# Performance work log

Hardware: AMD Instinct MI355X
Metric: run time of the kernel (lower is better)

## Reference

```python
import jax, jax.numpy as jnp
import numpy as np

CONF_THRES = 0.25   # NMS.conf
IOU_THRES = 0.45    # NMS.iou
MAX_NMS = 1024      # fixed candidate count so greedy NMS is jit-compatible
IMG = 640.0


def setup_inputs() -> dict:
    key = jax.random.key(0)
    k0, k1, k2, k3, k4 = jax.random.split(key, 5)
    B, N = 32, 25200
    cxcy = jax.random.uniform(k0, (B, N, 2), dtype=jnp.float32) * IMG
    wh = jax.random.uniform(k1, (B, N, 2), dtype=jnp.float32) * 80.0 + 2.0
    obj = jax.random.uniform(k2, (B, N, 1), dtype=jnp.float32)
    lmk = jax.random.uniform(k3, (B, N, 10), dtype=jnp.float32) * IMG
    cls = jax.random.uniform(k4, (B, N, 1), dtype=jnp.float32)
    # layout: [cx, cy, w, h, obj, 10 landmark coords, 1 class score]
    prediction = jnp.concatenate([cxcy, wh, obj, lmk, cls], axis=2)
    return {"prediction": prediction}


def xywh2xyxy(x):
    cx, cy, w, h = x[:, 0], x[:, 1], x[:, 2], x[:, 3]
    return jnp.stack([cx - w / 2, cy - h / 2, cx + w / 2, cy + h / 2], axis=1)


def pairwise_iou(b):  # b: [K,4] xyxy -> [K,K]
    area = (b[:, 2] - b[:, 0]) * (b[:, 3] - b[:, 1])
    lt = jnp.maximum(b[:, None, :2], b[None, :, :2])
    rb = jnp.minimum(b[:, None, 2:], b[None, :, 2:])
    wh = jnp.clip(rb - lt, 0.0)
    inter = wh[..., 0] * wh[..., 1]
    return inter / (area[:, None] + area[None, :] - inter + 1e-7)


def _nms_image(pred):  # pred: [N,16]
    obj = pred[:, 4]
    score = pred[:, 15] * obj  # x[:,15:] *= x[:,4:5]; nc==1 -> single class, j==0
    valid = (obj > CONF_THRES) & (score > CONF_THRES)  # xc filter + conf filter
    s = jnp.where(valid, score, -1.0)
    top_s, idx = jax.lax.top_k(s, MAX_NMS)  # score-sorted candidates (greedy NMS order)
    x = pred[idx]  # [K,16]
    box = xywh2xyxy(x[:, :4])
    vmask = top_s > 0.0  # valid candidates (invalid slots carry score -1)
    # class offset c = j*4096 is identically 0 since nc==1 -> skip
    iou = pairwise_iou(box)  # [K,K]
    rng = jnp.arange(MAX_NMS)

    def step(keep, i):
        sup = keep[i] & (iou[i] > IOU_THRES) & (rng > i)
        return keep & ~sup, None

    keep, _ = jax.lax.scan(step, vmask, rng)
    det = jnp.concatenate(
        [box, top_s[:, None], x[:, 5:15], jnp.zeros((MAX_NMS, 1), pred.dtype)], axis=1
    )  # [K,16] = box(4) | conf(1) | landmarks(10) | class(1)=0
    return det * keep[:, None].astype(det.dtype), keep


def reference(prediction):
    # Fixed-shape analogue of the per-image ragged output: detections padded to
    # MAX_NMS rows per image (zeroed where suppressed) plus a keep mask.
    det, keep = jax.vmap(_nms_image)(prediction)
    return det, keep
```

## Files before the change

### kernel.cpp

```cpp
#include <hip/hip_runtime.h>
#include <stdint.h>

#define NB 32
#define NN 25200
#define NN4 6300
#define TOPK 1024
#define NF 16
#define CONF 0.25f
#define IOU_T 0.45f
#define NBIN 4096
#define CAP 2048
#define KEY_BASE 0xBE800001u

__device__ __forceinline__ uint32_t score_key(float obj, float cls) {
  float score = __fmul_rn(cls, obj);
  bool valid = (obj > CONF) && (score > CONF);
  float s = valid ? score : -1.0f;
  uint32_t u = __float_as_uint(s);
  return (u & 0x80000000u) ? ~u : (u | 0x80000000u);
}

__device__ __forceinline__ uint64_t shfl_xor_u64(uint64_t v, int m) {
  uint32_t lo = __shfl_xor((uint32_t)v, m, 64);
  uint32_t hi = __shfl_xor((uint32_t)(v >> 32), m, 64);
  return ((uint64_t)hi << 32) | lo;
}

__global__ void k_keys(const float* __restrict__ pred, uint32_t* __restrict__ keys) {
  int g = blockIdx.x * blockDim.x + threadIdx.x;
  if (g >= NB * NN) return;
  const float* row = pred + (size_t)g * NF;
  keys[g] = score_key(row[4], row[15]);
}

__global__ __launch_bounds__(1024) void k_select(const uint32_t* __restrict__ keys,
                                                 int* __restrict__ sel) {
  int b = blockIdx.x;
  int tid = threadIdx.x;
  int lane = tid & 63, wid = tid >> 6;
  const uint4* kb4 = (const uint4*)(keys + (size_t)b * NN);
  __shared__ uint32_t hist[NBIN];
  __shared__ uint64_t ent[CAP];
  __shared__ uint32_t wsum[16];
  __shared__ uint32_t sh_bin;
  __shared__ uint32_t sh_cnt;
  #pragma unroll
  for (int k = 0; k < 4; ++k) hist[tid + 1024 * k] = 0;
  ent[tid] = 0; ent[tid + 1024] = 0;
  if (tid == 0) { sh_cnt = 0; sh_bin = 0; }
  __syncthreads();

  uint4 kreg[7];
  #pragma unroll
  for (int k = 0; k < 7; ++k) {
    int i = tid + k * 1024;
    if (i < NN4) {
      kreg[k] = kb4[i];
      uint32_t kv[4] = {kreg[k].x, kreg[k].y, kreg[k].z, kreg[k].w};
      #pragma unroll
      for (int c = 0; c < 4; ++c) {
        uint32_t key = kv[c];
        if (key >= KEY_BASE) {
          uint32_t bin = (key - KEY_BASE) >> 12;
          if (bin > NBIN - 1) bin = NBIN - 1;
          atomicAdd(&hist[bin], 1u);
        }
      }
    }
  }
  __syncthreads();

  uint32_t h[4]; uint32_t s = 0;
  #pragma unroll
  for (int k = 0; k < 4; ++k) { h[k] = hist[NBIN - 1 - (4 * tid + k)]; s += h[k]; }
  uint32_t my = s;
  #pragma unroll
  for (int d = 1; d < 64; d <<= 1) {
    uint32_t v = __shfl_up(s, d, 64);
    if (lane >= d) s += v;
  }
  if (lane == 63) wsum[wid] = s;
  __syncthreads();
  uint32_t base = 0;
  for (int w = 0; w < wid; ++w) base += wsum[w];
  uint32_t cum = base + s - my;
  #pragma unroll
  for (int k = 0; k < 4; ++k) {
    if (cum < TOPK && cum + h[k] >= TOPK) sh_bin = (uint32_t)(NBIN - 1 - (4 * tid + k));
    cum += h[k];
  }
  __syncthreads();
  uint32_t thr = KEY_BASE + (sh_bin << 12);

  #pragma unroll
  for (int k = 0; k < 7; ++k) {
    int i = tid + k * 1024;
    if (i < NN4) {
      uint32_t kv[4] = {kreg[k].x, kreg[k].y, kreg[k].z, kreg[k].w};
      #pragma unroll
      for (int c = 0; c < 4; ++c) {
        uint32_t key = kv[c];
        if (key >= thr) {
          uint32_t p = atomicAdd(&sh_cnt, 1u);
          if (p < CAP) ent[p] = ((uint64_t)key << 32) | (uint32_t)(~(uint32_t)(4 * i + c));
        }
      }
    }
  }
  __syncthreads();

  uint64_t v0 = ent[tid], v1 = ent[tid + 1024];
  for (unsigned kk = 2; kk <= CAP; kk <<= 1) {
    for (unsigned j = kk >> 1; j > 0; j >>= 1) {
      if (j == 1024) {
        uint64_t mx = v0 > v1 ? v0 : v1;
        uint64_t mn = v0 > v1 ? v1 : v0;
        v0 = mx; v1 = mn;
      } else if (j >= 64) {
        __syncthreads();
        ent[tid] = v0; ent[tid + 1024] = v1;
        __syncthreads();
        uint64_t p0 = ent[tid ^ j], p1 = ent[(tid ^ j) + 1024];
        bool low = ((tid & j) == 0);
        bool d0 = ((tid & kk) == 0);
        bool d1 = (((tid + 1024) & kk) == 0);
        v0 = (low != d0) ? (v0 < p0 ? v0 : p0) : (v0 > p0 ? v0 : p0);
        v1 = (low != d1) ? (v1 < p1 ? v1 : p1) : (v1 > p1 ? v1 : p1);
      } else {
        uint64_t p0 = shfl_xor_u64(v0, (int)j);
        uint64_t p1 = shfl_xor_u64(v1, (int)j);
        bool low = ((tid & j) == 0);
        bool d0 = ((tid & kk) == 0);
        bool d1 = (((tid + 1024) & kk) == 0);
        v0 = (low != d0) ? (v0 < p0 ? v0 : p0) : (v0 > p0 ? v0 : p0);
        v1 = (low != d1) ? (v1 < p1 ? v1 : p1) : (v1 > p1 ? v1 : p1);
      }
    }
  }
  uint32_t n = ~(uint32_t)(v0 & 0xFFFFFFFFu);
  if (n >= NN) n = 0;
  sel[(size_t)b * TOPK + tid] = (int)n;
}

__global__ __launch_bounds__(1024) void k_mask(const float* __restrict__ pred,
                                               const int* __restrict__ sel,
                                               uint32_t* __restrict__ mask) {
  int b = blockIdx.x;
  int sblk = blockIdx.y;
  int tid = threadIdx.x;
  int rg = tid & 31;
  int cc = tid >> 5;
  __shared__ float bx1[TOPK], by1[TOPK], bx2[TOPK], by2[TOPK], bar[TOPK];
  {
    int n = sel[(size_t)b * TOPK + tid];
    const float4* row = (const float4*)(pred + ((size_t)b * NN + n) * NF);
    float4 r0 = row[0];
    float hw = __fmul_rn(r0.z, 0.5f), hh = __fmul_rn(r0.w, 0.5f);
    float x1 = __fsub_rn(r0.x, hw), y1 = __fsub_rn(r0.y, hh);
    float x2 = __fadd_rn(r0.x, hw), y2 = __fadd_rn(r0.y, hh);
    bx1[tid] = x1; by1[tid] = y1; bx2[tid] = x2; by2[tid] = y2;
    bar[tid] = __fmul_rn(__fsub_rn(x2, x1), __fsub_rn(y2, y1));
  }
  __syncthreads();
  int i0 = sblk * 128 + rg * 4;
  int iw = i0 >> 5;
  uint32_t wreg[4] = {0u, 0u, 0u, 0u};
  if (cc >= iw) {
    float rx1[4], ry1[4], rx2[4], ry2[4], rar[4];
    #pragma unroll
    for (int k = 0; k < 4; ++k) {
      rx1[k] = bx1[i0 + k]; ry1[k] = by1[i0 + k];
      rx2[k] = bx2[i0 + k]; ry2[k] = by2[i0 + k]; rar[k] = bar[i0 + k];
    }
    for (int jj = 0; jj < 32; ++jj) {
      int j = cc * 32 + jj;
      float cx1 = bx1[j], cy1 = by1[j], cx2 = bx2[j], cy2 = by2[j], car = bar[j];
      #pragma unroll
      for (int k = 0; k < 4; ++k) {
        float lx = fmaxf(rx1[k], cx1);
        float ly = fmaxf(ry1[k], cy1);
        float rx = fminf(rx2[k], cx2);
        float ry = fminf(ry2[k], cy2);
        float wd = fmaxf(__fsub_rn(rx, lx), 0.0f);
        float ht = fmaxf(__fsub_rn(ry, ly), 0.0f);
        float inter = __fmul_rn(wd, ht);
        float den = __fadd_rn(__fsub_rn(__fadd_rn(rar[k], car), inter), 1e-7f);
        float iou = __fdiv_rn(inter, den);
        wreg[k] |= (iou > IOU_T ? 1u : 0u) << jj;
      }
    }
    if (cc == iw) {
      #pragma unroll
      for (int k = 0; k < 4; ++k)
        wreg[k] &= ~((2u << ((i0 + k) & 31)) - 1u);
    }
  }
  uint4 out = make_uint4(wreg[0], wreg[1], wreg[2], wreg[3]);
  *(uint4*)&mask[((size_t)b * 32 + cc) * TOPK + i0] = out;
}

__global__ __launch_bounds__(1024, 4) void k_scan_out(const float* __restrict__ pred,
                                                      const int* __restrict__ sel,
                                                      const uint32_t* __restrict__ mask,
                                                      float* __restrict__ det,
                                                      float* __restrict__ keep_out) {
  int b = blockIdx.x;
  int tid = threadIdx.x;
  int lane = tid & 63, wv = tid >> 6;
  __shared__ uint32_t vbits[32];
  __shared__ uint32_t keepw[32];

  uint32_t cur[32];
  const uint4* mc = nullptr;
  if (tid < 32) {
    mc = (const uint4*)(mask + (size_t)b * (32 * TOPK) + (size_t)tid * TOPK);
    #pragma unroll
    for (int q = 0; q < 8; ++q) *(uint4*)&cur[4 * q] = mc[q];
  }

  int n = sel[(size_t)b * TOPK + tid];
  const float4* rowv = (const float4*)(pred + ((size_t)b * NN + n) * NF);
  float4 r0 = rowv[0], r1 = rowv[1], r2 = rowv[2], r3 = rowv[3];
  float obj = r1.x, cls = r3.w;
  float score = __fmul_rn(cls, obj);
  bool valid = (obj > CONF) && (score > CONF);
  uint64_t bal = __ballot(valid);
  if (lane == 0) {
    vbits[2 * wv] = (uint32_t)bal;
    vbits[2 * wv + 1] = (uint32_t)(bal >> 32);
  }
  __syncthreads();

  if (tid < 32) {
    int l = tid;
    uint32_t kw = vbits[l];
    uint32_t nxt[32];
    for (int w = 0; w < 32; ++w) {
      if (w < 31) {
        #pragma unroll
        for (int q = 0; q < 8; ++q) *(uint4*)&nxt[4 * q] = mc[(w + 1) * 8 + q];
      }
      uint32_t rw = kw;
      #pragma unroll
      for (int t = 0; t < 32; ++t)
        if ((rw >> t) & 1u) rw &= ~cur[t];
      uint32_t rf = __shfl(rw, w, 64);
      if (l == w) {
        kw = rf;
      } else if (l > w) {
        uint32_t acc = 0;
        #pragma unroll
        for (int t = 0; t < 32; ++t) acc |= ((rf >> t) & 1u) ? cur[t] : 0u;
        kw &= ~acc;
      }
      if (w < 31) {
        #pragma unroll
        for (int t = 0; t < 32; ++t) cur[t] = nxt[t];
      }
    }
    keepw[l] = kw;
  }
  __syncthreads();

  bool kept = (keepw[tid >> 5] >> (tid & 31)) & 1u;
  float m = kept ? 1.0f : 0.0f;
  float hw = __fmul_rn(r0.z, 0.5f), hh = __fmul_rn(r0.w, 0.5f);
  float4 o0 = make_float4(__fsub_rn(r0.x, hw) * m, __fsub_rn(r0.y, hh) * m,
                          __fadd_rn(r0.x, hw) * m, __fadd_rn(r0.y, hh) * m);
  float4 o1 = make_float4(score * m, r1.y * m, r1.z * m, r1.w * m);
  float4 o2 = make_float4(r2.x * m, r2.y * m, r2.z * m, r2.w * m);
  float4 o3 = make_float4(r3.x * m, r3.y * m, r3.z * m, 0.0f);
  float4* dst = (float4*)(det + ((size_t)b * TOPK + tid) * NF);
  dst[0] = o0; dst[1] = o1; dst[2] = o2; dst[3] = o3;
  keep_out[(size_t)b * TOPK + tid] = m;
}

extern "C" void kernel_launch(void* const* d_in, const int* in_sizes, int n_in,
                              void* d_out, int out_size, void* d_ws, size_t ws_size,
                              hipStream_t stream) {
  const float* pred = (const float*)d_in[0];
  float* det = (float*)d_out;
  float* keep = det + (size_t)NB * TOPK * NF;

  uint8_t* ws = (uint8_t*)d_ws;
  uint32_t* keys = (uint32_t*)ws;
  int* sel = (int*)(ws + (size_t)NB * NN * 4);
  uint32_t* mask = (uint32_t*)(ws + (size_t)NB * NN * 4
                                  + (size_t)NB * TOPK * 4);

  k_keys<<<(NB * NN + 255) / 256, 256, 0, stream>>>(pred, keys);
  k_select<<<NB, 1024, 0, stream>>>(keys, sel);
  dim3 gm(NB, 8);
  k_mask<<<gm, 1024, 0, stream>>>(pred, sel, mask);
  k_scan_out<<<NB, 1024, 0, stream>>>(pred, sel, mask, det, keep);
}
```

Baseline: 167.3 us.

## Fuse IoU mask and greedy scan kernels using per-image atomic counter handoff

```diff
diff --git a/kernel.cpp b/kernel.cpp
--- a/kernel.cpp
+++ b/kernel.cpp
@@ -26,7 +26,9 @@
   return ((uint64_t)hi << 32) | lo;
 }
 
-__global__ void k_keys(const float* __restrict__ pred, uint32_t* __restrict__ keys) {
+__global__ void k_keys(const float* __restrict__ pred, uint32_t* __restrict__ keys,
+                       uint32_t* __restrict__ cnt) {
+  if (blockIdx.x == 0 && threadIdx.x < NB) cnt[threadIdx.x] = 0u;
   int g = blockIdx.x * blockDim.x + threadIdx.x;
   if (g >= NB * NN) return;
   const float* row = pred + (size_t)g * NF;
@@ -142,15 +144,21 @@
   sel[(size_t)b * TOPK + tid] = (int)n;
 }
 
-__global__ __launch_bounds__(1024) void k_mask(const float* __restrict__ pred,
-                                               const int* __restrict__ sel,
-                                               uint32_t* __restrict__ mask) {
+__global__ __launch_bounds__(1024, 4) void k_maskscan(const float* __restrict__ pred,
+                                                      const int* __restrict__ sel,
+                                                      uint32_t* __restrict__ mask,
+                                                      uint32_t* __restrict__ cnt,
+                                                      float* __restrict__ det,
+                                                      float* __restrict__ keep_out) {
   int b = blockIdx.x;
   int sblk = blockIdx.y;
   int tid = threadIdx.x;
   int rg = tid & 31;
   int cc = tid >> 5;
   __shared__ float bx1[TOPK], by1[TOPK], bx2[TOPK], by2[TOPK], bar[TOPK];
+  __shared__ uint32_t vbits[32];
+  __shared__ uint32_t keepw[32];
+
   {
     int n = sel[(size_t)b * TOPK + tid];
     const float4* row = (const float4*)(pred + ((size_t)b * NN + n) * NF);
@@ -197,26 +205,17 @@
   }
   uint4 out = make_uint4(wreg[0], wreg[1], wreg[2], wreg[3]);
   *(uint4*)&mask[((size_t)b * 32 + cc) * TOPK + i0] = out;
-}
-
-__global__ __launch_bounds__(1024, 4) void k_scan_out(const float* __restrict__ pred,
-                                                      const int* __restrict__ sel,
-                                                      const uint32_t* __restrict__ mask,
-                                                      float* __restrict__ det,
-                                                      float* __restrict__ keep_out) {
-  int b = blockIdx.x;
-  int tid = threadIdx.x;
+
+  __threadfence();
+  __syncthreads();
+  if (tid == 0)
+    __hip_atomic_fetch_add(&cnt[b], 1u, __ATOMIC_RELEASE, __HIP_MEMORY_SCOPE_AGENT);
+  if (sblk != 0) return;
+
   int lane = tid & 63, wv = tid >> 6;
-  __shared__ uint32_t vbits[32];
-  __shared__ uint32_t keepw[32];
-
-  uint32_t cur[32];
   const uint4* mc = nullptr;
-  if (tid < 32) {
+  if (tid < 32)
     mc = (const uint4*)(mask + (size_t)b * (32 * TOPK) + (size_t)tid * TOPK);
-    #pragma unroll
-    for (int q = 0; q < 8; ++q) *(uint4*)&cur[4 * q] = mc[q];
-  }
 
   int n = sel[(size_t)b * TOPK + tid];
   const float4* rowv = (const float4*)(pred + ((size_t)b * NN + n) * NF);
@@ -231,8 +230,18 @@
   }
   __syncthreads();
 
+  if (tid == 0) {
+    while (__hip_atomic_load(&cnt[b], __ATOMIC_ACQUIRE, __HIP_MEMORY_SCOPE_AGENT) < 8u)
+      __builtin_amdgcn_s_sleep(2);
+  }
+  __syncthreads();
+
   if (tid < 32) {
+    (void)__hip_atomic_load(&cnt[b], __ATOMIC_ACQUIRE, __HIP_MEMORY_SCOPE_AGENT);
     int l = tid;
+    uint32_t cur[32];
+    #pragma unroll
+    for (int q = 0; q < 8; ++q) *(uint4*)&cur[4 * q] = mc[q];
     uint32_t kw = vbits[l];
     uint32_t nxt[32];
     for (int w = 0; w < 32; ++w) {
@@ -287,10 +296,12 @@
   int* sel = (int*)(ws + (size_t)NB * NN * 4);
   uint32_t* mask = (uint32_t*)(ws + (size_t)NB * NN * 4
                                   + (size_t)NB * TOPK * 4);
-
-  k_keys<<<(NB * NN + 255) / 256, 256, 0, stream>>>(pred, keys);
+  uint32_t* cnt = (uint32_t*)(ws + (size_t)NB * NN * 4
+                                 + (size_t)NB * TOPK * 4
+                                 + (size_t)NB * 32 * TOPK * 4);
+
+  k_keys<<<(NB * NN + 255) / 256, 256, 0, stream>>>(pred, keys, cnt);
   k_select<<<NB, 1024, 0, stream>>>(keys, sel);
   dim3 gm(NB, 8);
-  k_mask<<<gm, 1024, 0, stream>>>(pred, sel, mask);
-  k_scan_out<<<NB, 1024, 0, stream>>>(pred, sel, mask, det, keep);
-}
+  k_maskscan<<<gm, 1024, 0, stream>>>(pred, sel, mask, cnt, det, keep);
+}
```

Measured after the change: 224.8 us. 34.4% more time.
